# Performance work log

Hardware: AMD Instinct MI355X
Metric: run time of the kernel (lower is better)

Reference implementation:

```python
import jax, jax.numpy as jnp
import numpy as np

PERMS = ((0, 1, 2, 3), (2, 1, 3, 0), (3, 1, 0, 2))


def setup_inputs() -> dict:
    key = jax.random.key(0)
    ks = jax.random.split(key, 10)
    N_n1, F = 50000, 128
    N_imp = 100000
    H = 512
    h = jax.random.normal(ks[0], (N_n1, F), dtype=jnp.float32)
    idx = jax.random.randint(ks[1], (N_imp, 4), 0, N_n1, dtype=jnp.int64)
    s = 0.05
    W1 = jax.random.normal(ks[2], (4 * F, H), dtype=jnp.float32) * s
    b1 = jax.random.normal(ks[3], (H,), dtype=jnp.float32) * s
    W2 = jax.random.normal(ks[4], (H, H), dtype=jnp.float32) * s
    b2 = jax.random.normal(ks[5], (H,), dtype=jnp.float32) * s
    W3 = jax.random.normal(ks[6], (H, H), dtype=jnp.float32) * s
    b3 = jax.random.normal(ks[7], (H,), dtype=jnp.float32) * s
    Wo = jax.random.normal(ks[8], (H, 2), dtype=jnp.float32) * s
    bo = jax.random.normal(ks[9], (2,), dtype=jnp.float32) * s
    return {"h": h, "idx": idx, "W1": W1, "b1": b1, "W2": W2, "b2": b2,
            "W3": W3, "b3": b3, "Wo": Wo, "bo": bo}


def reference(h, idx, W1, b1, W2, b2, W3, b3, Wo, bo):
    # Message passing: copy_u + mean over exactly one edge per relation == gather.
    hi = h[idx]  # [N, 4, F]
    N = hi.shape[0]
    # Stack the 3 permutations of the 4 neighbor features: [3, N, 4F]
    x = jnp.stack([hi[:, jnp.array(p), :].reshape(N, -1) for p in PERMS], axis=0)
    # Shared MLP (config = [512, relu] x 3), broadcast over permutation axis.
    x = jax.nn.relu(x @ W1 + b1)
    x = jax.nn.relu(x @ W2 + b2)
    x = jax.nn.relu(x @ W3 + b3)
    pooled = jnp.sum(x, axis=0)  # Janossy sum over permutations: [N, 512]
    return pooled @ Wo + bo  # [N, 2]
```

## Files before the change

kernel.cpp:

```cpp
#include <hip/hip_runtime.h>
#include <stdint.h>
#include <stddef.h>


typedef __attribute__((ext_vector_type(8))) short short8;
typedef __attribute__((ext_vector_type(16))) float f32x16;
typedef __attribute__((ext_vector_type(4))) float floatv4;
typedef __attribute__((ext_vector_type(8))) unsigned short ushort8;

#define GLOAD_LDS16(g, l)                                                      \
  __builtin_amdgcn_global_load_lds(                                            \
      (const __attribute__((address_space(1))) void*)(g),                      \
      (__attribute__((address_space(3))) void*)(l), 16, 0, 0)

__device__ __forceinline__ unsigned short f2bf(float f) {
  unsigned int u = __float_as_uint(f);
  u += 0x7fffu + ((u >> 16) & 1u);
  return (unsigned short)(u >> 16);
}
__device__ __forceinline__ float bf2f(unsigned short s) {
  return __uint_as_float(((unsigned int)s) << 16);
}

#define NNODES 100000
#define MTOT   300000
#define HD     512
#define NH     50000
#define LSTR   152

__global__ __launch_bounds__(256) void prep_w(const float* __restrict__ W1,
                                              const float* __restrict__ W2,
                                              const float* __restrict__ W3,
                                              unsigned short* __restrict__ Wt) {
  int t = blockIdx.x * 256 + threadIdx.x;
  int layer = t >> 18;
  int r = t & 262143;
  int e = r & 7;
  int q16 = r >> 3;
  int s = q16 & 1023;
  int blk = q16 >> 10;
  int nb = blk >> 3, kt = blk & 7;
  int c = ((s >> 8) << 1) | ((s >> 5) & 1);
  int row = ((s >> 6) & 3) * 32 + (s & 31);
  int n = nb * 128 + row;
  int k = kt * 64 + c * 8 + e;
  const float* W = layer == 0 ? W1 : (layer == 1 ? W2 : W3);
  Wt[t] = f2bf(W[k * 512 + n]);
}

__global__ __launch_bounds__(256) void prep_hb(const float* __restrict__ h,
                                               unsigned short* __restrict__ hb) {
  int t = blockIdx.x * 256 + threadIdx.x;
  int v = t >> 4, c8 = (t & 15) * 8;
  const floatv4* hp = (const floatv4*)(h + (size_t)v * 128 + c8);
  floatv4 f0 = hp[0], f1 = hp[1];
  ushort8 o;
#pragma unroll
  for (int e = 0; e < 4; ++e) {
    o[e] = f2bf(f0[e]);
    o[4 + e] = f2bf(f1[e]);
  }
  *(ushort8*)(hb + (size_t)v * 128 + c8) = o;
}

__global__ __launch_bounds__(256) void init_out(float* __restrict__ out,
                                                const float* __restrict__ bo) {
  int t = blockIdx.x * 256 + threadIdx.x;
  if (t < 2 * NNODES) out[t] = bo[t & 1];
}

template <int GATHER, int FINAL>
__global__ __launch_bounds__(256, 4) void gemm_k(
    const unsigned short* __restrict__ A,
    const int* __restrict__ idx,
    const unsigned short* __restrict__ Wt,
    const float* __restrict__ bias,
    unsigned short* __restrict__ Xout,
    float* __restrict__ out, const float* __restrict__ Wo,
    int mchunk0) {
  __shared__ __align__(16) char smem[39936];
  char* sB = smem;
  char* sA = smem + 16384;
  int* sIdx = (int*)(smem + 32768);
  float* sWo = (float*)(smem + 38912);

  const int t = threadIdx.x;
  int bx = blockIdx.x;
  int xcd = bx & 7, tq = bx >> 3;
  int cbk = tq & 3;
  int rb = xcd + ((tq >> 2) << 3);
  int n0 = cbk * 128;
  int rb8 = rb * 8;
  int w = t >> 6, l = t & 63;
  int wmq = (w >> 1) * 2, wnq = (w & 1) * 2;
  int m32 = l & 31, half = l >> 5;
  int wm = wmq * 32;

  if (GATHER) {
    if (t < 128) {
      int m = mchunk0 + rb * 128 + t;
      unsigned um = (unsigned)m;
      unsigned n = um / 3u;
      int p = (int)(um - n * 3u);
      if (n >= NNODES) n = 0;
      const unsigned pk0 = 0x320u, pk1 = 0x111u, pk2 = 0x032u, pk3 = 0x203u;
      int sh = p * 4;
      sIdx[t * 4 + 0] = idx[n * 4 + ((pk0 >> sh) & 0xFu)];
      sIdx[t * 4 + 1] = idx[n * 4 + ((pk1 >> sh) & 0xFu)];
      sIdx[t * 4 + 2] = idx[n * 4 + ((pk2 >> sh) & 0xFu)];
      sIdx[t * 4 + 3] = idx[n * 4 + ((pk3 >> sh) & 0xFu)];
    }
    __syncthreads();
  }

  f32x16 acc[2][2];
#pragma unroll
  for (int i = 0; i < 2; ++i)
#pragma unroll
    for (int j = 0; j < 2; ++j)
#pragma unroll
      for (int r = 0; r < 16; ++r) acc[i][j][r] = 0.f;

  for (int kt = 0; kt < 8; ++kt) {
    short8 afr[4][2];
    if (!GATHER) {
      const unsigned short* ga = A + ((size_t)(rb8 + kt) * 1024) * 8;
#pragma unroll
      for (int ks = 0; ks < 4; ++ks)
#pragma unroll
        for (int i = 0; i < 2; ++i)
          afr[ks][i] = *(const short8*)(ga +
              (size_t)(ks * 256 + (wmq + i) * 64 + l) * 8);
    }
    {
      const unsigned short* gb = Wt + ((size_t)(cbk * 8 + kt) * 1024 + t) * 8;
#pragma unroll
      for (int i = 0; i < 4; ++i)
        GLOAD_LDS16(gb + (size_t)i * 2048, sB + (i * 256 + t) * 16);
    }
    if (GATHER) {
      int jblk = kt >> 1;
      int inner = (kt & 1) * 64;
#pragma unroll
      for (int i = 0; i < 4; ++i) {
        int s = i * 256 + t;
        int r = s >> 3;
        int cl = (s & 7) ^ (r & 7);
        int src = sIdx[r * 4 + jblk];
        GLOAD_LDS16(A + (size_t)src * 128 + inner + cl * 8, sA + s * 16);
      }
    }
    __syncthreads();
#pragma unroll
    for (int ks = 0; ks < 4; ++ks) {
      short8 bfr[2];
#pragma unroll
      for (int j = 0; j < 2; ++j)
        bfr[j] = *(const short8*)(sB + (ks * 256 + (wnq + j) * 64 + l) * 16);
      if (GATHER) {
        short8 ag[2];
        int cbp = ((ks << 1) + half) ^ (m32 & 7);
#pragma unroll
        for (int i = 0; i < 2; ++i)
          ag[i] = *(const short8*)(sA + (wm + i * 32 + m32) * 128 + cbp * 16);
#pragma unroll
        for (int i = 0; i < 2; ++i)
#pragma unroll
          for (int j = 0; j < 2; ++j)
            acc[i][j] = __builtin_amdgcn_mfma_f32_32x32x16_bf16(
                ag[i], bfr[j], acc[i][j], 0, 0, 0);
      } else {
#pragma unroll
        for (int i = 0; i < 2; ++i)
#pragma unroll
          for (int j = 0; j < 2; ++j)
            acc[i][j] = __builtin_amdgcn_mfma_f32_32x32x16_bf16(
                afr[ks][i], bfr[j], acc[i][j], 0, 0, 0);
      }
    }
    __syncthreads();
  }

  unsigned short* L = (unsigned short*)smem;
  if (FINAL && t < 256) sWo[t] = Wo[n0 * 2 + t];
#pragma unroll
  for (int i = 0; i < 2; ++i)
#pragma unroll
    for (int j = 0; j < 2; ++j) {
      int coll = wnq * 32 + j * 32 + m32;
      float bv = bias[n0 + coll];
#pragma unroll
      for (int r = 0; r < 16; ++r) {
        int rowl = wm + i * 32 + (r & 3) + 8 * (r >> 2) + 4 * half;
        float v = fmaxf(acc[i][j][r] + bv, 0.f);
        L[rowl * LSTR + coll] = f2bf(v);
      }
    }
  __syncthreads();

  if (!FINAL) {
#pragma unroll
    for (int v = 0; v < 8; ++v) {
      int chunk = v * 256 + t;
      int ktsel = chunk >> 10;
      int s = chunk & 1023;
      int ks_l = s >> 8;
      int rowhi = (s >> 6) & 3;
      int hb_ = (s >> 5) & 1;
      int row = rowhi * 32 + (s & 31);
      int col_local = ktsel * 64 + (((ks_l << 1) | hb_) << 3);
      ushort8 val = *(const ushort8*)(L + row * LSTR + col_local);
      *(ushort8*)(Xout + ((size_t)(rb8 + 2 * cbk + ktsel) * 1024 + s) * 8) = val;
    }
  } else {
    int r2 = t >> 1, jo = t & 1;
    int grow = mchunk0 + rb * 128 + r2;
    if (grow < MTOT) {
      const unsigned short* Lr = L + r2 * LSTR;
      float s = 0.f;
#pragma unroll
      for (int cc = 0; cc < 128; cc += 2) {
        unsigned int pair = *(const unsigned int*)(Lr + cc);
        s += bf2f((unsigned short)(pair & 0xffffu)) * sWo[2 * cc + jo];
        s += bf2f((unsigned short)(pair >> 16)) * sWo[2 * cc + 2 + jo];
      }
      int node = grow / 3;
      atomicAdd(out + node * 2 + jo, s);
    }
  }
}

extern "C" void kernel_launch(void* const* d_in, const int* in_sizes, int n_in,
                              void* d_out, int out_size, void* d_ws,
                              size_t ws_size, hipStream_t stream) {
  const float* h  = (const float*)d_in[0];
  const int*   ix = (const int*)d_in[1];
  const float* W1 = (const float*)d_in[2];
  const float* b1 = (const float*)d_in[3];
  const float* W2 = (const float*)d_in[4];
  const float* b2 = (const float*)d_in[5];
  const float* W3 = (const float*)d_in[6];
  const float* b3 = (const float*)d_in[7];
  const float* Wo = (const float*)d_in[8];
  const float* bo = (const float*)d_in[9];
  float* out = (float*)d_out;

  unsigned short* ws = (unsigned short*)d_ws;
  unsigned short* Wt = ws;
  unsigned short* hb = Wt + 786432;
  unsigned short* bufs = hb + 6400000;
  const size_t baseBytes = (786432ull + 6400000ull) * 2;

  size_t avail = ws_size > baseBytes ? ws_size - baseBytes : 0;
  size_t ncap = avail / (2ull * 3 * HD * sizeof(unsigned short));
  size_t nc = (ncap / 2048) * 2048;
  if (nc > 32768) nc = 32768;
  if (nc == 0) nc = 2048;
  unsigned short* X1 = bufs;
  unsigned short* X2 = X1 + nc * 3 * HD;

  prep_w<<<3072, 256, 0, stream>>>(W1, W2, W3, Wt);
  prep_hb<<<NH * 16 / 256, 256, 0, stream>>>(h, hb);
  init_out<<<(2 * NNODES + 255) / 256, 256, 0, stream>>>(out, bo);

  for (size_t n0c = 0; n0c < NNODES; n0c += nc) {
    size_t remn = (size_t)NNODES - n0c;
    size_t ncp = remn < nc ? ((remn + 2047) / 2048) * 2048 : nc;
    int rows = (int)(ncp * 3);
    int RB = rows / 128;
    int m0 = (int)(3 * n0c);
    gemm_k<1, 0><<<RB * 4, 256, 0, stream>>>(hb, ix, Wt, b1, X1, nullptr,
                                             nullptr, m0);
    gemm_k<0, 0><<<RB * 4, 256, 0, stream>>>(X1, nullptr, Wt + 262144, b2, X2,
                                             nullptr, nullptr, m0);
    gemm_k<0, 1><<<RB * 4, 256, 0, stream>>>(X2, nullptr, Wt + 524288, b3,
                                             nullptr, out, Wo, m0);
  }
}
```

Measured before the change: 652.9 us.

## Double-buffer gathered A tiles and load B fragments directly from global

The gather path now double-buffers the A tile in LDS, issuing the next k-tile's gather while MFMAs run on the current one, and drops one barrier per iteration. Both paths stop staging the weight tile through LDS and instead load pre-swizzled B fragments straight from global into registers. The non-gather path preloads all A and B fragments for a k-step before its MFMAs. Launch bounds drop from 4 to 3 blocks per SM to make room for the extra registers, which reduces occupancy, and loading B per wave duplicates global traffic across waves.

```diff
diff --git a/kernel.cpp b/kernel.cpp
--- a/kernel.cpp
+++ b/kernel.cpp
@@ -70,7 +70,7 @@
 }
 
 template <int GATHER, int FINAL>
-__global__ __launch_bounds__(256, 4) void gemm_k(
+__global__ __launch_bounds__(256, 3) void gemm_k(
     const unsigned short* __restrict__ A,
     const int* __restrict__ idx,
     const unsigned short* __restrict__ Wt,
@@ -78,10 +78,11 @@
     unsigned short* __restrict__ Xout,
     float* __restrict__ out, const float* __restrict__ Wo,
     int mchunk0) {
-  __shared__ __align__(16) char smem[39936];
-  char* sB = smem;
-  char* sA = smem + 16384;
-  int* sIdx = (int*)(smem + 32768);
+  constexpr int SMEM = GATHER ? 40960 : 39936;
+  __shared__ __align__(16) char smem[SMEM];
+  char* sA0 = smem;
+  char* sA1 = smem + 16384;
+  int* sIdx = (int*)(smem + 38912);
   float* sWo = (float*)(smem + 38912);
 
   const int t = threadIdx.x;
@@ -95,6 +96,19 @@
   int wmq = (w >> 1) * 2, wnq = (w & 1) * 2;
   int m32 = l & 31, half = l >> 5;
   int wm = wmq * 32;
+
+  auto stageA = [&](int ktv, char* buf) {
+    int jblk = ktv >> 1;
+    int inner = (ktv & 1) * 64;
+#pragma unroll
+    for (int i = 0; i < 4; ++i) {
+      int s = i * 256 + t;
+      int r = s >> 3;
+      int cl = (s & 7) ^ (r & 7);
+      int src = sIdx[r * 4 + jblk];
+      GLOAD_LDS16(A + (size_t)src * 128 + inner + cl * 8, buf + s * 16);
+    }
+  };
 
   if (GATHER) {
     if (t < 128) {
@@ -121,68 +135,67 @@
 #pragma unroll
       for (int r = 0; r < 16; ++r) acc[i][j][r] = 0.f;
 
-  for (int kt = 0; kt < 8; ++kt) {
-    short8 afr[4][2];
-    if (!GATHER) {
-      const unsigned short* ga = A + ((size_t)(rb8 + kt) * 1024) * 8;
+  const unsigned short* Bbase = Wt + (size_t)(cbk * 8) * 1024 * 8;
+
+  if (!GATHER) {
+    const unsigned short* Abase = A + (size_t)rb8 * 1024 * 8;
+#pragma unroll
+    for (int kt = 0; kt < 8; ++kt) {
+      short8 afr[8], bfr[8];
 #pragma unroll
       for (int ks = 0; ks < 4; ++ks)
 #pragma unroll
+        for (int i = 0; i < 2; ++i) {
+          afr[ks * 2 + i] = *(const short8*)(
+              Abase + ((size_t)kt * 1024 + ks * 256 + (wmq + i) * 64 + l) * 8);
+          bfr[ks * 2 + i] = *(const short8*)(
+              Bbase + ((size_t)kt * 1024 + ks * 256 + (wnq + i) * 64 + l) * 8);
+        }
+#pragma unroll
+      for (int ks = 0; ks < 4; ++ks)
+#pragma unroll
         for (int i = 0; i < 2; ++i)
-          afr[ks][i] = *(const short8*)(ga +
-              (size_t)(ks * 256 + (wmq + i) * 64 + l) * 8);
-    }
-    {
-      const unsigned short* gb = Wt + ((size_t)(cbk * 8 + kt) * 1024 + t) * 8;
-#pragma unroll
-      for (int i = 0; i < 4; ++i)
-        GLOAD_LDS16(gb + (size_t)i * 2048, sB + (i * 256 + t) * 16);
-    }
-    if (GATHER) {
-      int jblk = kt >> 1;
-      int inner = (kt & 1) * 64;
-#pragma unroll
-      for (int i = 0; i < 4; ++i) {
-        int s = i * 256 + t;
-        int r = s >> 3;
-        int cl = (s & 7) ^ (r & 7);
-        int src = sIdx[r * 4 + jblk];
-        GLOAD_LDS16(A + (size_t)src * 128 + inner + cl * 8, sA + s * 16);
-      }
-    }
-    __syncthreads();
-#pragma unroll
-    for (int ks = 0; ks < 4; ++ks) {
-      short8 bfr[2];
-#pragma unroll
-      for (int j = 0; j < 2; ++j)
-        bfr[j] = *(const short8*)(sB + (ks * 256 + (wnq + j) * 64 + l) * 16);
-      if (GATHER) {
+#pragma unroll
+          for (int j = 0; j < 2; ++j)
+            acc[i][j] = __builtin_amdgcn_mfma_f32_32x32x16_bf16(
+                afr[ks * 2 + i], bfr[ks * 2 + j], acc[i][j], 0, 0, 0);
+    }
+  } else {
+    stageA(0, sA0);
+#pragma unroll
+    for (int kt = 0; kt < 8; ++kt) {
+      char* curA = (kt & 1) ? sA1 : sA0;
+      char* nxtA = (kt & 1) ? sA0 : sA1;
+      __syncthreads();
+      if (kt < 7) stageA(kt + 1, nxtA);
+      short8 bfr[8];
+#pragma unroll
+      for (int ks = 0; ks < 4; ++ks)
+#pragma unroll
+        for (int j = 0; j < 2; ++j)
+          bfr[ks * 2 + j] = *(const short8*)(
+              Bbase + ((size_t)kt * 1024 + ks * 256 + (wnq + j) * 64 + l) * 8);
+#pragma unroll
+      for (int ks = 0; ks < 4; ++ks) {
         short8 ag[2];
         int cbp = ((ks << 1) + half) ^ (m32 & 7);
 #pragma unroll
         for (int i = 0; i < 2; ++i)
-          ag[i] = *(const short8*)(sA + (wm + i * 32 + m32) * 128 + cbp * 16);
+          ag[i] = *(const short8*)(curA + (wm + i * 32 + m32) * 128 + cbp * 16);
 #pragma unroll
         for (int i = 0; i < 2; ++i)
 #pragma unroll
           for (int j = 0; j < 2; ++j)
             acc[i][j] = __builtin_amdgcn_mfma_f32_32x32x16_bf16(
-                ag[i], bfr[j], acc[i][j], 0, 0, 0);
-      } else {
-#pragma unroll
-        for (int i = 0; i < 2; ++i)
-#pragma unroll
-          for (int j = 0; j < 2; ++j)
-            acc[i][j] = __builtin_amdgcn_mfma_f32_32x32x16_bf16(
-                afr[ks][i], bfr[j], acc[i][j], 0, 0, 0);
+                ag[i], bfr[ks * 2 + j], acc[i][j], 0, 0, 0);
       }
     }
-    __syncthreads();
-  }
+  }
+
+  if (FINAL && t < 256) sWo[t] = Wo[n0 * 2 + t];
+  __syncthreads();
 
   unsigned short* L = (unsigned short*)smem;
-  if (FINAL && t < 256) sWo[t] = Wo[n0 * 2 + t];
 #pragma unroll
   for (int i = 0; i < 2; ++i)
 #pragma unroll
```

Measured after the change: 835.8 us. 1.28x slower.

## Double-buffer weight tiles in LDS for non-gather GEMM layers

Applied to the files above, without the earlier changes.

For the non-gather layers, the weight tile is now staged into two alternating LDS buffers. The next k-tile is prefetched while MFMAs run on the current one, which drops one barrier per iteration and hides global-to-LDS latency. The gather path keeps single buffering, and an extra barrier is added before the epilogue so the Wo load and LDS reuse stay safe. The cost is 16KB more LDS for B in the non-gather path, reusing the region that held A, plus full unrolling of the k-loop.

```diff
diff --git a/kernel.cpp b/kernel.cpp
--- a/kernel.cpp
+++ b/kernel.cpp
@@ -79,8 +79,8 @@
     float* __restrict__ out, const float* __restrict__ Wo,
     int mchunk0) {
   __shared__ __align__(16) char smem[39936];
-  char* sB = smem;
-  char* sA = smem + 16384;
+  char* sB0 = smem;
+  char* sB1 = smem + 16384;
   int* sIdx = (int*)(smem + 32768);
   float* sWo = (float*)(smem + 38912);
 
@@ -95,6 +95,25 @@
   int wmq = (w >> 1) * 2, wnq = (w & 1) * 2;
   int m32 = l & 31, half = l >> 5;
   int wm = wmq * 32;
+
+  auto stageB = [&](int ktv, char* buf) {
+    const unsigned short* gbp = Wt + ((size_t)(cbk * 8 + ktv) * 1024 + t) * 8;
+#pragma unroll
+    for (int i = 0; i < 4; ++i)
+      GLOAD_LDS16(gbp + (size_t)i * 2048, buf + (i * 256 + t) * 16);
+  };
+  auto stageA = [&](int ktv, char* buf) {
+    int jblk = ktv >> 1;
+    int inner = (ktv & 1) * 64;
+#pragma unroll
+    for (int i = 0; i < 4; ++i) {
+      int s = i * 256 + t;
+      int r = s >> 3;
+      int cl = (s & 7) ^ (r & 7);
+      int src = sIdx[r * 4 + jblk];
+      GLOAD_LDS16(A + (size_t)src * 128 + inner + cl * 8, buf + s * 16);
+    }
+  };
 
   if (GATHER) {
     if (t < 128) {
@@ -121,43 +140,50 @@
 #pragma unroll
       for (int r = 0; r < 16; ++r) acc[i][j][r] = 0.f;
 
-  for (int kt = 0; kt < 8; ++kt) {
-    short8 afr[4][2];
-    if (!GATHER) {
-      const unsigned short* ga = A + ((size_t)(rb8 + kt) * 1024) * 8;
+  if (!GATHER) {
+    const unsigned short* Abase = A + (size_t)rb8 * 1024 * 8;
+    stageB(0, sB0);
+#pragma unroll
+    for (int kt = 0; kt < 8; ++kt) {
+      char* curB = (kt & 1) ? sB1 : sB0;
+      char* nxtB = (kt & 1) ? sB0 : sB1;
+      short8 afr[8];
 #pragma unroll
       for (int ks = 0; ks < 4; ++ks)
 #pragma unroll
         for (int i = 0; i < 2; ++i)
-          afr[ks][i] = *(const short8*)(ga +
-              (size_t)(ks * 256 + (wmq + i) * 64 + l) * 8);
-    }
-    {
-      const unsigned short* gb = Wt + ((size_t)(cbk * 8 + kt) * 1024 + t) * 8;
-#pragma unroll
-      for (int i = 0; i < 4; ++i)
-        GLOAD_LDS16(gb + (size_t)i * 2048, sB + (i * 256 + t) * 16);
-    }
-    if (GATHER) {
-      int jblk = kt >> 1;
-      int inner = (kt & 1) * 64;
-#pragma unroll
-      for (int i = 0; i < 4; ++i) {
-        int s = i * 256 + t;
-        int r = s >> 3;
-        int cl = (s & 7) ^ (r & 7);
-        int src = sIdx[r * 4 + jblk];
-        GLOAD_LDS16(A + (size_t)src * 128 + inner + cl * 8, sA + s * 16);
+          afr[ks * 2 + i] = *(const short8*)(
+              Abase + ((size_t)kt * 1024 + ks * 256 + (wmq + i) * 64 + l) * 8);
+      __syncthreads();
+      if (kt < 7) stageB(kt + 1, nxtB);
+#pragma unroll
+      for (int ks = 0; ks < 4; ++ks) {
+        short8 bfr[2];
+#pragma unroll
+        for (int j = 0; j < 2; ++j)
+          bfr[j] =
+              *(const short8*)(curB + (ks * 256 + (wnq + j) * 64 + l) * 16);
+#pragma unroll
+        for (int i = 0; i < 2; ++i)
+#pragma unroll
+          for (int j = 0; j < 2; ++j)
+            acc[i][j] = __builtin_amdgcn_mfma_f32_32x32x16_bf16(
+                afr[ks * 2 + i], bfr[j], acc[i][j], 0, 0, 0);
       }
     }
-    __syncthreads();
-#pragma unroll
-    for (int ks = 0; ks < 4; ++ks) {
-      short8 bfr[2];
-#pragma unroll
-      for (int j = 0; j < 2; ++j)
-        bfr[j] = *(const short8*)(sB + (ks * 256 + (wnq + j) * 64 + l) * 16);
-      if (GATHER) {
+  } else {
+    char* sB = sB0;
+    char* sA = sB1;
+    for (int kt = 0; kt < 8; ++kt) {
+      stageA(kt, sA);
+      stageB(kt, sB);
+      __syncthreads();
+#pragma unroll
+      for (int ks = 0; ks < 4; ++ks) {
+        short8 bfr[2];
+#pragma unroll
+        for (int j = 0; j < 2; ++j)
+          bfr[j] = *(const short8*)(sB + (ks * 256 + (wnq + j) * 64 + l) * 16);
         short8 ag[2];
         int cbp = ((ks << 1) + half) ^ (m32 & 7);
 #pragma unroll
@@ -169,20 +195,15 @@
           for (int j = 0; j < 2; ++j)
             acc[i][j] = __builtin_amdgcn_mfma_f32_32x32x16_bf16(
                 ag[i], bfr[j], acc[i][j], 0, 0, 0);
-      } else {
-#pragma unroll
-        for (int i = 0; i < 2; ++i)
-#pragma unroll
-          for (int j = 0; j < 2; ++j)
-            acc[i][j] = __builtin_amdgcn_mfma_f32_32x32x16_bf16(
-                afr[ks][i], bfr[j], acc[i][j], 0, 0, 0);
       }
-    }
-    __syncthreads();
-  }
+      __syncthreads();
+    }
+  }
+
+  if (FINAL && t < 256) sWo[t] = Wo[n0 * 2 + t];
+  __syncthreads();
 
   unsigned short* L = (unsigned short*)smem;
-  if (FINAL && t < 256) sWo[t] = Wo[n0 * 2 + t];
 #pragma unroll
   for (int i = 0; i < 2; ++i)
 #pragma unroll
```

Measured after the change: 699.7 us. 7.2% more time.
